# Optimization experiments

Hardware: AMD Instinct MI355X
Metric: run time of the kernel (lower is better)

The kernel has to match this reference:

```python
import jax, jax.numpy as jnp
import numpy as np

HIDDEN = 1024
HEADS = 16
HEAD_DIM = HIDDEN // HEADS
RANK = 256
B, S = 4, 2048


def setup_inputs() -> dict:
    key = jax.random.key(0)
    ks = jax.random.split(key, 10)
    sc_in = 1.0 / np.sqrt(HIDDEN)
    sc_r = 1.0 / np.sqrt(RANK)
    inp = {"hidden_states": jax.random.normal(ks[0], (B, S, HIDDEN), dtype=jnp.float32)}
    names = ["q", "k", "v"]
    for i, n in enumerate(names):
        inp[f"{n}A"] = jax.random.normal(ks[1 + 3 * i], (HIDDEN, RANK), dtype=jnp.float32) * sc_in
        inp[f"{n}B"] = jax.random.normal(ks[2 + 3 * i], (RANK, HIDDEN), dtype=jnp.float32) * sc_r
        inp[f"{n}b"] = jnp.zeros((HIDDEN,), dtype=jnp.float32)
    return inp


def _split_heads(x):
    # [B,S,H*D] -> [B,H,S,D]
    Bh, Sh, _ = x.shape
    return x.reshape(Bh, Sh, HEADS, HEAD_DIM).transpose(0, 2, 1, 3)


def reference(hidden_states, qA, qB, qb, kA, kB, kb, vA, vB, vb):
    # Low-rank projections: x @ A @ B + b (factorized linear)
    q = hidden_states @ qA @ qB + qb
    k = hidden_states @ kA @ kB + kb
    v = hidden_states @ vA @ vB + vb
    q = _split_heads(q)  # [B,H,S,D]
    k = _split_heads(k)
    v = _split_heads(v)
    scores = jnp.einsum("bhqd,bhkd->bhqk", q, k) / np.sqrt(HEAD_DIM)
    probs = jax.nn.softmax(scores, axis=-1)  # dropout is identity at inference
    ctx = jnp.einsum("bhqk,bhkd->bhqd", probs, v)
    ctx = ctx.transpose(0, 2, 1, 3).reshape(hidden_states.shape[0], hidden_states.shape[1], HIDDEN)
    return ctx
```

## Files before the change

### kernel.cpp

```cpp
#include <hip/hip_runtime.h>


typedef unsigned short u16;
typedef unsigned int   u32;
typedef __attribute__((ext_vector_type(4)))  float    f32x4;
typedef __attribute__((ext_vector_type(16))) float    f32x16;
typedef __attribute__((ext_vector_type(8)))  short    short8;
typedef __attribute__((ext_vector_type(8)))  _Float16 half8;
typedef __attribute__((ext_vector_type(4)))  u16      u16x4;

#define HID 1024
#define R_  256
#define S_  2048
#define B_  4
#define H_  16
#define D_  64
#define M_  (B_ * S_)

#define BM 128
#define BN 64
#define BK 64
#define LDP 72

#define KVB 64
#define SCL 0.18033688011112f
#define MSHIFT 8.0f

__device__ __forceinline__ u16 f2h(float f) {
    _Float16 h = (_Float16)f;
    return __builtin_bit_cast(u16, h);
}
__device__ __forceinline__ u32 pkrtz(float a, float b) {
    auto r = __builtin_amdgcn_cvt_pkrtz(a, b);
    return __builtin_bit_cast(u32, r);
}

__device__ __forceinline__ f32x4 mfma16(short8 a, short8 b, f32x4 c) {
    return __builtin_amdgcn_mfma_f32_16x16x32_f16(
        __builtin_bit_cast(half8, a), __builtin_bit_cast(half8, b), c, 0, 0, 0);
}
__device__ __forceinline__ f32x16 mfma32(short8 a, short8 b, f32x16 c) {
    return __builtin_amdgcn_mfma_f32_32x32x16_f16(
        __builtin_bit_cast(half8, a), __builtin_bit_cast(half8, b), c, 0, 0, 0);
}

__device__ __forceinline__ void gload16(const u16* g, u16* l) {
    __builtin_amdgcn_global_load_lds(
        (__attribute__((address_space(1))) const void*)g,
        (__attribute__((address_space(3))) void*)l,
        16, 0, 0);
}

#if defined(__has_builtin)
#if __has_builtin(__builtin_amdgcn_permlane32_swap)
#define HAVE_PLSWAP 1
#endif
#endif
__device__ __forceinline__ void plswap(u32 x, u32 y, u32& lo, u32& hi) {
#ifdef HAVE_PLSWAP
    typedef __attribute__((ext_vector_type(2))) unsigned uv2;
    uv2 r = __builtin_amdgcn_permlane32_swap(x, y, false, false);
    lo = r.x; hi = r.y;
#else
    u32 ty = (u32)__shfl_xor((int)y, 32);
    u32 tx = (u32)__shfl_xor((int)x, 32);
    int h = (threadIdx.x & 63) >> 5;
    lo = h ? ty : x;
    hi = h ? y : tx;
#endif
}

__global__ __launch_bounds__(256) void cvt_hs_kernel(const float* __restrict__ src,
                                                     u16* __restrict__ dst) {
    int i = (blockIdx.x * 256 + threadIdx.x) * 4;
    float4 v = *(const float4*)(src + i);
    u16x4 u;
    u[0] = f2h(v.x); u[1] = f2h(v.y); u[2] = f2h(v.z); u[3] = f2h(v.w);
    *(u16x4*)(dst + i) = u;
}

__global__ __launch_bounds__(256) void pack_weights_kernel(
    const float* __restrict__ qA, const float* __restrict__ kA, const float* __restrict__ vA,
    const float* __restrict__ qB, const float* __restrict__ kB, const float* __restrict__ vB,
    u16* __restrict__ At, u16* __restrict__ Bt) {
    int which = blockIdx.y;
    int o = blockIdx.x * 256 + threadIdx.x;
    if (which < 3) {
        const float* src = (which == 0) ? qA : (which == 1) ? kA : vA;
        u16* dst = At + (size_t)which * R_ * HID;
        int c = o >> 10, r = o & 1023;
        dst[o] = f2h(src[(size_t)r * R_ + c]);
    } else {
        int w = which - 3;
        const float* src = (w == 0) ? qB : (w == 1) ? kB : vB;
        float scl = (w == 0) ? SCL : 1.0f;
        u16* dst = Bt + (size_t)w * HID * R_;
        int c = o >> 8, r = o & 255;
        dst[o] = f2h(src[(size_t)r * HID + c] * scl);
    }
}

template <int KDIM, int NOUT, bool QKV_OUT>
__global__ __launch_bounds__(256, 3) void gemm_kernel(
    const u16* __restrict__ X, const u16* __restrict__ Wt, u16* __restrict__ Y,
    const float* __restrict__ bq, const float* __restrict__ bk, const float* __restrict__ bv) {
    const int w  = blockIdx.z;
    const int m0 = blockIdx.x * BM;
    const int n0 = blockIdx.y * BN;
    const u16* Xp = X + (QKV_OUT ? (size_t)w * M_ * KDIM : (size_t)0);
    const u16* Wp = Wt + (size_t)w * NOUT * KDIM;
    u16* Yp = Y + (size_t)w * M_ * NOUT;
    const float* bias = nullptr;
    float bscl = 1.0f;
    if constexpr (QKV_OUT) { bias = (w == 0) ? bq : (w == 1) ? bk : bv; bscl = (w == 0) ? SCL : 1.0f; }

    __shared__ __align__(16) u16 As[2][BM * BK];
    __shared__ __align__(16) u16 Bs[2][BN * BK];

    const int tid  = threadIdx.x;
    const int lane = tid & 63, wv = tid >> 6;
    const int l16 = lane & 15, lg = lane >> 4;
    const int wrow = (wv >> 1) * 64, wcol = (wv & 1) * 32;

    const int sr = lane >> 3, sp = lane & 7, sc = sp ^ sr;

#define G_STAGE(bf, k0)                                                       \
    {                                                                         \
        _Pragma("unroll")                                                     \
        for (int j = 0; j < 4; ++j) {                                         \
            int ra = wv * 32 + j * 8;                                         \
            gload16(Xp + (size_t)(m0 + ra + sr) * KDIM + (k0) + sc * 8,       \
                    &As[bf][ra * 64]);                                        \
        }                                                                     \
        _Pragma("unroll")                                                     \
        for (int j = 0; j < 2; ++j) {                                         \
            int rb = wv * 16 + j * 8;                                         \
            gload16(Wp + (size_t)(n0 + rb + sr) * KDIM + (k0) + sc * 8,       \
                    &Bs[bf][rb * 64]);                                        \
        }                                                                     \
    }

    f32x4 acc[4][2];
#pragma unroll
    for (int i = 0; i < 4; ++i)
#pragma unroll
        for (int j = 0; j < 2; ++j) acc[i][j] = (f32x4){0.f, 0.f, 0.f, 0.f};

    G_STAGE(0, 0);
    int cur = 0;
    for (int k0 = 0; k0 < KDIM; k0 += BK) {
        __syncthreads();
        if (k0 + BK < KDIM) G_STAGE(cur ^ 1, k0 + BK);
        const u16* ab = &As[cur][0];
        const u16* bb = &Bs[cur][0];
        __builtin_amdgcn_s_setprio(1);
#pragma unroll
        for (int ks = 0; ks < 2; ++ks) {
            short8 af[4], bf[2];
#pragma unroll
            for (int ri = 0; ri < 4; ++ri) {
                int r = wrow + ri * 16 + l16;
                int c = ks * 4 + lg;
                af[ri] = *(const short8*)(ab + r * 64 + ((c ^ (r & 7)) * 8));
            }
#pragma unroll
            for (int ci = 0; ci < 2; ++ci) {
                int r = wcol + ci * 16 + l16;
                int c = ks * 4 + lg;
                bf[ci] = *(const short8*)(bb + r * 64 + ((c ^ (r & 7)) * 8));
            }
#pragma unroll
            for (int ri = 0; ri < 4; ++ri)
#pragma unroll
                for (int ci = 0; ci < 2; ++ci)
                    acc[ri][ci] = mfma16(af[ri], bf[ci], acc[ri][ci]);
        }
        __builtin_amdgcn_s_setprio(0);
        cur ^= 1;
    }
#undef G_STAGE
#pragma unroll
    for (int ri = 0; ri < 4; ++ri)
#pragma unroll
        for (int ci = 0; ci < 2; ++ci)
#pragma unroll
            for (int i = 0; i < 4; ++i) {
                int r = m0 + wrow + ri * 16 + lg * 4 + i;
                int c = n0 + wcol + ci * 16 + l16;
                float val = acc[ri][ci][i];
                if constexpr (QKV_OUT) val += bias[c] * bscl;
                Yp[(size_t)r * NOUT + c] = f2h(val);
            }
}

__global__ __launch_bounds__(256) void vtrans_kernel(const u16* __restrict__ v,
                                                     u16* __restrict__ vT) {
    int s0 = blockIdx.x * 64;
    int bh = blockIdx.y;
    int b = bh >> 4, h = bh & 15;
    __shared__ __align__(16) u16 tl[64][LDP];
    int t = threadIdx.x;
    int r = t >> 2;
#pragma unroll
    for (int i = 0; i < 2; ++i) {
        int c = i * 32 + (t & 3) * 8;
        *(short8*)&tl[r][c] = *(const short8*)(v + (size_t)(b * S_ + s0 + r) * HID + h * D_ + c);
    }
    __syncthreads();
    int d = t >> 2;
#pragma unroll
    for (int i = 0; i < 2; ++i) {
        int sb = i * 32 + (t & 3) * 8;
        short8 o;
#pragma unroll
        for (int j = 0; j < 8; ++j) o[j] = (short)tl[sb + j][d];
        *(short8*)(vT + ((size_t)bh * D_ + d) * S_ + s0 + sb) = o;
    }
}

__global__ __launch_bounds__(256) void attn_kernel(
    const u16* __restrict__ Q, const u16* __restrict__ K,
    const u16* __restrict__ VT, float* __restrict__ out) {
    const int f = blockIdx.x;
    const int xcd = f & 7, idx = f >> 3;
    const int bh = xcd * 8 + (idx >> 4);
    const int qt = idx & 15;
    const int b = bh >> 4, h = bh & 15;
    const int tid = threadIdx.x, lane = tid & 63, wv = tid >> 6;
    const int l31 = lane & 31, hi = lane >> 5;
    const int q0 = qt * 128 + wv * 32;
    const int rx = l31 & 7;

    __shared__ __align__(16) u16 Ks[2][KVB * 64];
    __shared__ __align__(16) u16 Vs[2][KVB * 64];

    short8 qf[4];
    {
        const u16* qp = Q + ((size_t)(b * S_ + q0 + l31)) * HID + h * D_ + 8 * hi;
#pragma unroll
        for (int ks = 0; ks < 4; ++ks) qf[ks] = *(const short8*)(qp + 16 * ks);
    }

    f32x16 ctx0, ctx1;
#pragma unroll
    for (int i = 0; i < 16; ++i) { ctx0[i] = 0.f; ctx1[i] = 0.f; }
    float la0 = 0.f, la1 = 0.f, la2 = 0.f, la3 = 0.f;

    const u16* Kg = K + (size_t)(b * S_) * HID + h * D_;
    const u16* Vg = VT + (size_t)bh * D_ * S_;
    const int sr = lane >> 3, sp = lane & 7, sc = sp ^ sr;

#define STAGE_ATTN(bf, kv0)                                                  \
    {                                                                        \
        _Pragma("unroll")                                                    \
        for (int j = 0; j < 2; ++j) {                                        \
            int rg = wv * 16 + j * 8;                                        \
            gload16(Kg + (size_t)((kv0) + rg + sr) * HID + sc * 8,           \
                    &Ks[bf][rg * 64]);                                       \
            gload16(Vg + (size_t)(rg + sr) * S_ + (kv0) + sc * 8,            \
                    &Vs[bf][rg * 64]);                                       \
        }                                                                    \
    }

    STAGE_ATTN(0, 0);
    int cur = 0;
    for (int t = 0; t < S_ / KVB; ++t) {
        __syncthreads();
        if (t + 1 < S_ / KVB) STAGE_ATTN(cur ^ 1, (t + 1) * KVB);

        f32x16 p0, p1;
#pragma unroll
        for (int i = 0; i < 16; ++i) { p0[i] = -MSHIFT; p1[i] = -MSHIFT; }
        const u16* kb = &Ks[cur][0];
        __builtin_amdgcn_s_setprio(1);
#pragma unroll
        for (int ks = 0; ks < 4; ++ks) {
            int sl = (2 * ks + hi) ^ rx;
            short8 a0 = *(const short8*)(kb + l31 * 64 + sl * 8);
            short8 a1 = *(const short8*)(kb + (32 + l31) * 64 + sl * 8);
            p0 = mfma32(a0, qf[ks], p0);
            p1 = mfma32(a1, qf[ks], p1);
        }
        __builtin_amdgcn_s_setprio(0);

#pragma unroll
        for (int i = 0; i < 16; ++i) {
            p0[i] = __builtin_amdgcn_exp2f(p0[i]);
            p1[i] = __builtin_amdgcn_exp2f(p1[i]);
        }
#pragma unroll
        for (int i = 0; i < 4; ++i) {
            la0 += p0[i] + p0[4 + i];
            la1 += p0[8 + i] + p0[12 + i];
            la2 += p1[i] + p1[4 + i];
            la3 += p1[8 + i] + p1[12 + i];
        }

        short8 pa[4];
#define PACK_CHUNK(pv, base, dst)                                   \
        {                                                           \
            u32 x0 = pkrtz(pv[base + 0], pv[base + 1]);             \
            u32 x1 = pkrtz(pv[base + 2], pv[base + 3]);             \
            u32 x2 = pkrtz(pv[base + 4], pv[base + 5]);             \
            u32 x3 = pkrtz(pv[base + 6], pv[base + 7]);             \
            u32 w0, w1, w2, w3;                                     \
            plswap(x0, x2, w0, w2);                                 \
            plswap(x1, x3, w1, w3);                                 \
            union { u32 w[4]; short8 v; } uu;                       \
            uu.w[0] = w0; uu.w[1] = w1; uu.w[2] = w2; uu.w[3] = w3; \
            dst = uu.v;                                             \
        }
        PACK_CHUNK(p0, 0, pa[0]);
        PACK_CHUNK(p0, 8, pa[1]);
        PACK_CHUNK(p1, 0, pa[2]);
        PACK_CHUNK(p1, 8, pa[3]);
#undef PACK_CHUNK

        const u16* vb = &Vs[cur][0];
        __builtin_amdgcn_s_setprio(1);
#pragma unroll
        for (int c = 0; c < 4; ++c) {
            int sl = (2 * c + hi) ^ rx;
            short8 v0 = *(const short8*)(vb + l31 * 64 + sl * 8);
            short8 v1 = *(const short8*)(vb + (32 + l31) * 64 + sl * 8);
            ctx0 = mfma32(v0, pa[c], ctx0);
            ctx1 = mfma32(v1, pa[c], ctx1);
        }
        __builtin_amdgcn_s_setprio(0);
        cur ^= 1;
    }
#undef STAGE_ATTN

    float l = (la0 + la1) + (la2 + la3);
    l += __shfl_xor(l, 32);
    float invl = 1.0f / l;
    float* op = out + ((size_t)(b * S_ + q0 + l31)) * HID + h * D_;
#pragma unroll
    for (int g = 0; g < 4; ++g) {
        f32x4 o0, o1;
#pragma unroll
        for (int i = 0; i < 4; ++i) {
            o0[i] = ctx0[4 * g + i] * invl;
            o1[i] = ctx1[4 * g + i] * invl;
        }
        *(f32x4*)(op + 8 * g + 4 * hi) = o0;
        *(f32x4*)(op + 32 + 8 * g + 4 * hi) = o1;
    }
}

extern "C" void kernel_launch(void* const* d_in, const int* in_sizes, int n_in,
                              void* d_out, int out_size, void* d_ws, size_t ws_size,
                              hipStream_t stream) {
    const float* hs = (const float*)d_in[0];
    const float* qA = (const float*)d_in[1];
    const float* qB = (const float*)d_in[2];
    const float* qb = (const float*)d_in[3];
    const float* kA = (const float*)d_in[4];
    const float* kB = (const float*)d_in[5];
    const float* kb = (const float*)d_in[6];
    const float* vA = (const float*)d_in[7];
    const float* vB = (const float*)d_in[8];
    const float* vb = (const float*)d_in[9];

    char* ws = (char*)d_ws;
    size_t off = 0;
    u16* hsb = (u16*)(ws + off); off += (size_t)M_ * HID * 2;
    u16* At  = (u16*)(ws + off); off += (size_t)3 * R_ * HID * 2;
    u16* Bt  = (u16*)(ws + off); off += (size_t)3 * HID * R_ * 2;
    u16* T   = (u16*)(ws + off); off += (size_t)3 * M_ * R_ * 2;
    u16* QKV = (u16*)(ws + off); off += (size_t)3 * M_ * HID * 2;
    u16* VT  = (u16*)(ws + off);

    cvt_hs_kernel<<<dim3((M_ * HID) / 1024), 256, 0, stream>>>(hs, hsb);
    pack_weights_kernel<<<dim3(1024, 6), 256, 0, stream>>>(qA, kA, vA, qB, kB, vB, At, Bt);

    gemm_kernel<HID, R_, false><<<dim3(M_ / BM, R_ / BN, 3), 256, 0, stream>>>(
        hsb, At, T, nullptr, nullptr, nullptr);
    gemm_kernel<R_, HID, true><<<dim3(M_ / BM, HID / BN, 3), 256, 0, stream>>>(
        T, Bt, QKV, qb, kb, vb);

    vtrans_kernel<<<dim3(S_ / 64, B_ * H_), 256, 0, stream>>>(QKV + (size_t)2 * M_ * HID, VT);
    attn_kernel<<<dim3(S_ / 8 / 16 * 64), 256, 0, stream>>>(
        QKV, QKV + (size_t)M_ * HID, VT, (float*)d_out);
}
```

Baseline: 160.4 us.

## Fuse V transpose into projection GEMM epilogue and merge prep kernels

```diff
diff --git a/kernel.cpp b/kernel.cpp
--- a/kernel.cpp
+++ b/kernel.cpp
@@ -20,7 +20,6 @@
 #define BM 128
 #define BN 64
 #define BK 64
-#define LDP 72
 
 #define KVB 64
 #define SCL 0.18033688011112f
@@ -70,21 +69,23 @@
 #endif
 }
 
-__global__ __launch_bounds__(256) void cvt_hs_kernel(const float* __restrict__ src,
-                                                     u16* __restrict__ dst) {
-    int i = (blockIdx.x * 256 + threadIdx.x) * 4;
-    float4 v = *(const float4*)(src + i);
-    u16x4 u;
-    u[0] = f2h(v.x); u[1] = f2h(v.y); u[2] = f2h(v.z); u[3] = f2h(v.w);
-    *(u16x4*)(dst + i) = u;
-}
-
-__global__ __launch_bounds__(256) void pack_weights_kernel(
+__global__ __launch_bounds__(256) void prep_kernel(
+    const float* __restrict__ hs, u16* __restrict__ hsb,
     const float* __restrict__ qA, const float* __restrict__ kA, const float* __restrict__ vA,
     const float* __restrict__ qB, const float* __restrict__ kB, const float* __restrict__ vB,
     u16* __restrict__ At, u16* __restrict__ Bt) {
-    int which = blockIdx.y;
-    int o = blockIdx.x * 256 + threadIdx.x;
+    int bx = blockIdx.x;
+    if (bx < 8192) {
+        int i = (bx * 256 + threadIdx.x) * 4;
+        float4 v = *(const float4*)(hs + i);
+        u16x4 u;
+        u[0] = f2h(v.x); u[1] = f2h(v.y); u[2] = f2h(v.z); u[3] = f2h(v.w);
+        *(u16x4*)(hsb + i) = u;
+        return;
+    }
+    int pb = bx - 8192;
+    int which = pb >> 10;
+    int o = (pb & 1023) * 256 + threadIdx.x;
     if (which < 3) {
         const float* src = (which == 0) ? qA : (which == 1) ? kA : vA;
         u16* dst = At + (size_t)which * R_ * HID;
@@ -103,6 +104,7 @@
 template <int KDIM, int NOUT, bool QKV_OUT>
 __global__ __launch_bounds__(256, 3) void gemm_kernel(
     const u16* __restrict__ X, const u16* __restrict__ Wt, u16* __restrict__ Y,
+    u16* __restrict__ Yv,
     const float* __restrict__ bq, const float* __restrict__ bk, const float* __restrict__ bv) {
     const int w  = blockIdx.z;
     const int m0 = blockIdx.x * BM;
@@ -153,7 +155,6 @@
         if (k0 + BK < KDIM) G_STAGE(cur ^ 1, k0 + BK);
         const u16* ab = &As[cur][0];
         const u16* bb = &Bs[cur][0];
-        __builtin_amdgcn_s_setprio(1);
 #pragma unroll
         for (int ks = 0; ks < 2; ++ks) {
             short8 af[4], bf[2];
@@ -175,10 +176,29 @@
                 for (int ci = 0; ci < 2; ++ci)
                     acc[ri][ci] = mfma16(af[ri], bf[ci], acc[ri][ci]);
         }
-        __builtin_amdgcn_s_setprio(0);
         cur ^= 1;
     }
 #undef G_STAGE
+
+    if constexpr (QKV_OUT) {
+        if (w == 2) {
+            const int bq_ = m0 >> 11;
+            const int s_base = (m0 & 2047) + wrow + lg * 4;
+#pragma unroll
+            for (int ci = 0; ci < 2; ++ci) {
+                int c = n0 + wcol + ci * 16 + l16;
+                int h = c >> 6, d = c & 63;
+                u16* colp = Yv + (((size_t)(bq_ * 16 + h) * 64 + d) << 11);
+                float bi = bias[c];
+#pragma unroll
+                for (int ri = 0; ri < 4; ++ri)
+#pragma unroll
+                    for (int i = 0; i < 4; ++i)
+                        colp[s_base + ri * 16 + i] = f2h(acc[ri][ci][i] + bi);
+            }
+            return;
+        }
+    }
 #pragma unroll
     for (int ri = 0; ri < 4; ++ri)
 #pragma unroll
@@ -191,31 +211,6 @@
                 if constexpr (QKV_OUT) val += bias[c] * bscl;
                 Yp[(size_t)r * NOUT + c] = f2h(val);
             }
-}
-
-__global__ __launch_bounds__(256) void vtrans_kernel(const u16* __restrict__ v,
-                                                     u16* __restrict__ vT) {
-    int s0 = blockIdx.x * 64;
-    int bh = blockIdx.y;
-    int b = bh >> 4, h = bh & 15;
-    __shared__ __align__(16) u16 tl[64][LDP];
-    int t = threadIdx.x;
-    int r = t >> 2;
-#pragma unroll
-    for (int i = 0; i < 2; ++i) {
-        int c = i * 32 + (t & 3) * 8;
-        *(short8*)&tl[r][c] = *(const short8*)(v + (size_t)(b * S_ + s0 + r) * HID + h * D_ + c);
-    }
-    __syncthreads();
-    int d = t >> 2;
-#pragma unroll
-    for (int i = 0; i < 2; ++i) {
-        int sb = i * 32 + (t & 3) * 8;
-        short8 o;
-#pragma unroll
-        for (int j = 0; j < 8; ++j) o[j] = (short)tl[sb + j][d];
-        *(short8*)(vT + ((size_t)bh * D_ + d) * S_ + s0 + sb) = o;
-    }
 }
 
 __global__ __launch_bounds__(256) void attn_kernel(
@@ -272,7 +267,6 @@
 #pragma unroll
         for (int i = 0; i < 16; ++i) { p0[i] = -MSHIFT; p1[i] = -MSHIFT; }
         const u16* kb = &Ks[cur][0];
-        __builtin_amdgcn_s_setprio(1);
 #pragma unroll
         for (int ks = 0; ks < 4; ++ks) {
             int sl = (2 * ks + hi) ^ rx;
@@ -281,7 +275,6 @@
             p0 = mfma32(a0, qf[ks], p0);
             p1 = mfma32(a1, qf[ks], p1);
         }
-        __builtin_amdgcn_s_setprio(0);
 
 #pragma unroll
         for (int i = 0; i < 16; ++i) {
@@ -317,7 +310,6 @@
 #undef PACK_CHUNK
 
         const u16* vb = &Vs[cur][0];
-        __builtin_amdgcn_s_setprio(1);
 #pragma unroll
         for (int c = 0; c < 4; ++c) {
             int sl = (2 * c + hi) ^ rx;
@@ -326,7 +318,6 @@
             ctx0 = mfma32(v0, pa[c], ctx0);
             ctx1 = mfma32(v1, pa[c], ctx1);
         }
-        __builtin_amdgcn_s_setprio(0);
         cur ^= 1;
     }
 #undef STAGE_ATTN
@@ -371,15 +362,13 @@
     u16* QKV = (u16*)(ws + off); off += (size_t)3 * M_ * HID * 2;
     u16* VT  = (u16*)(ws + off);
 
-    cvt_hs_kernel<<<dim3((M_ * HID) / 1024), 256, 0, stream>>>(hs, hsb);
-    pack_weights_kernel<<<dim3(1024, 6), 256, 0, stream>>>(qA, kA, vA, qB, kB, vB, At, Bt);
+    prep_kernel<<<dim3(8192 + 6144), 256, 0, stream>>>(hs, hsb, qA, kA, vA, qB, kB, vB, At, Bt);
 
     gemm_kernel<HID, R_, false><<<dim3(M_ / BM, R_ / BN, 3), 256, 0, stream>>>(
-        hsb, At, T, nullptr, nullptr, nullptr);
+        hsb, At, T, nullptr, nullptr, nullptr, nullptr);
     gemm_kernel<R_, HID, true><<<dim3(M_ / BM, HID / BN, 3), 256, 0, stream>>>(
-        T, Bt, QKV, qb, kb, vb);
-
-    vtrans_kernel<<<dim3(S_ / 64, B_ * H_), 256, 0, stream>>>(QKV + (size_t)2 * M_ * HID, VT);
-    attn_kernel<<<dim3(S_ / 8 / 16 * 64), 256, 0, stream>>>(
+        T, Bt, QKV, VT, qb, kb, vb);
+
+    attn_kernel<<<dim3(1024), 256, 0, stream>>>(
         QKV, QKV + (size_t)M_ * HID, VT, (float*)d_out);
 }
```

New measurement: 155.5 us. 3.1% less time.
